# Performance work log

Hardware: AMD Instinct MI355X
Metric: run time of the kernel (lower is better)

The kernel has to match this reference:

```python
import jax, jax.numpy as jnp
import numpy as np

B, T, N, F, CH = 64, 8, 2000, 16, 64  # batch, timesteps(=receptive field), nodes, in features, channels (h_dim//2)
TASK = CH          # task_dim = h_dim // 2
P_TREAT = 0.5      # args.p
P1 = 1.0           # args.p1
BN_EPS = 1e-5


def setup_inputs() -> dict:
    key = jax.random.key(0)
    ks = jax.random.split(key, 40)
    def rn(i, shape, s=0.1):
        return jax.random.normal(ks[i], shape, dtype=jnp.float32) * s
    return {
        "X": jax.random.normal(ks[0], (B, T, N, F), dtype=jnp.float32),
        "A": jax.random.uniform(ks[1], (N, N), dtype=jnp.float32),
        "C": jax.random.randint(ks[2], (B, N), 0, 2, dtype=jnp.int32),
        "Y": jax.random.uniform(ks[3], (B, N), dtype=jnp.float32),
        "Cc": jnp.zeros((B, N), jnp.float32),
        "start_w": rn(4, (CH, F)),
        "start_b": rn(5, (CH,), 0.01),
        "filt_w": rn(6, (3, CH, CH, 2)),
        "filt_b": rn(7, (3, CH), 0.01),
        "gate_w": rn(8, (3, CH, CH, 2)),
        "gate_b": rn(9, (3, CH), 0.01),
        "skip_w": rn(10, (3, CH, CH)),
        "skip_b": rn(11, (3, CH), 0.01),
        "bn_g": 1.0 + rn(12, (3, CH), 0.01),
        "bn_b": rn(13, (3, CH), 0.01),
        "nodevec1": jax.random.normal(ks[14], (N, 10), dtype=jnp.float32),
        "nodevec2": jax.random.normal(ks[15], (10, N), dtype=jnp.float32),
        "task_emb": rn(16, (TASK,)),
        "gcn_w": rn(17, (CH, 3 * CH)),
        "gcn_b": rn(18, (CH,), 0.01),
        "h0_w1": rn(19, (CH, TASK + CH)),
        "h0_b1": rn(20, (CH,), 0.01),
        "h0_w2": rn(21, (1, CH)),
        "h0_b2": rn(22, (1,), 0.01),
        "h1_w1": rn(23, (CH, TASK + CH)),
        "h1_b1": rn(24, (CH,), 0.01),
        "h1_w2": rn(25, (1, CH)),
        "h1_b2": rn(26, (1,), 0.01),
    }


def _conv1x1(x, w, b):
    # x: (B,Cin,N,L), w: (Cout,Cin)
    return jnp.einsum('bcnl,oc->bonl', x, w) + b[None, :, None, None]


def _dil_conv(x, w, b, d):
    # kernel (1,2), dilation d along time, no padding -> width shrinks by d
    L = x.shape[-1]
    y = (jnp.einsum('bcnl,oc->bonl', x[..., :L - d], w[:, :, 0])
         + jnp.einsum('bcnl,oc->bonl', x[..., d:], w[:, :, 1]))
    return y + b[None, :, None, None]


def reference(X, A, C, Y, Cc, start_w, start_b, filt_w, filt_b, gate_w, gate_b,
              skip_w, skip_b, bn_g, bn_b, nodevec1, nodevec2, task_emb, gcn_w, gcn_b,
              h0_w1, h0_b1, h0_w2, h0_b2, h1_w1, h1_b1, h1_w2, h1_b2):
    x = jnp.transpose(X, (0, 3, 2, 1))            # (B,F,N,T)
    x = _conv1x1(x, start_w, start_b)             # (B,CH,N,T)
    adp = jax.nn.softmax(jax.nn.relu(nodevec1 @ nodevec2), axis=1)  # (N,N)
    skip = None
    d = 1
    for i in range(3):  # layers, dilations 1,2,4
        res = x
        f = jnp.tanh(_dil_conv(res, filt_w[i], filt_b[i], d))
        g = jax.nn.sigmoid(_dil_conv(res, gate_w[i], gate_b[i], d))
        x = f * g
        s = _conv1x1(x, skip_w[i], skip_b[i])
        skip = s if skip is None else s + skip[..., -s.shape[-1]:]
        x = x + res[..., -x.shape[-1]:]
        # eval-mode BatchNorm2d with running_mean=0, running_var=1
        scale = (bn_g[i] / jnp.sqrt(1.0 + BN_EPS))[None, :, None, None]
        x = x * scale + bn_b[i][None, :, None, None]
        d *= 2
    # gcn on skip (width 1): out = [x, A@x, A@(A@x)] -> concat -> 1x1 (dropout=eval identity)
    x1 = jnp.einsum('bcvl,vw->bcwl', skip, adp)
    x2 = jnp.einsum('bcvl,vw->bcwl', x1, adp)
    h = jnp.concatenate([skip, x1, x2], axis=1)   # (B,3CH,N,1)
    gx = jax.nn.relu(_conv1x1(h, gcn_w, gcn_b))   # (B,CH,N,1)
    bs, _, n_nodes, _ = gx.shape
    task = jnp.broadcast_to(task_emb[None, :, None, None], (bs, TASK, n_nodes, 1))
    z = jnp.concatenate([task, gx], axis=1)       # (B,TASK+CH,N,1)

    def hyp(w1, b1, w2, b2):
        hh = jax.nn.relu(_conv1x1(z, w1, b1))
        return _conv1x1(hh, w2, b2).reshape(-1)

    y1 = jax.nn.sigmoid(hyp(h1_w1, h1_b1, h1_w2, h1_b2))
    y0 = jax.nn.sigmoid(hyp(h0_w1, h0_b1, h0_w2, h0_b2))
    t = C.reshape(-1)
    y = jnp.where(t > 0, y1, y0)
    yc = jnp.clip(y, 1e-7, 1.0 - 1e-7)
    Yf = Y.reshape(-1)
    bce = -jnp.mean(Yf * jnp.log(yc) + (1.0 - Yf) * jnp.log(1.0 - yc))
    # linear MMD (mmd2_lin, CFR): masked means, jit-friendly
    zb = jnp.transpose(z, (0, 2, 1, 3)).reshape(bs * n_nodes, -1)  # (B*N, TASK+CH)
    tm = (t > 0).astype(zb.dtype)
    mean_t = (tm @ zb) / jnp.maximum(tm.sum(), 1.0)
    mean_c = ((1.0 - tm) @ zb) / jnp.maximum((1.0 - tm).sum(), 1.0)
    imb = jnp.sum((2.0 * P_TREAT * mean_t - 2.0 * (1.0 - P_TREAT) * mean_c) ** 2)
    loss = bce + P1 * imb
    return (loss, y, y0, y1)
```

## Files before the change

### kernel.cpp

```cpp
#include <hip/hip_runtime.h>
#include <cstdint>

#define NB 64
#define TT 8
#define NN 2000
#define NF 16
#define NCH 64
#define NPAD 2048
#define BCD 4096
#define ITEMS 128000

#define OFF_ADPF  0
#define OFF_ST    4194304
#define OFF_X2    0
#define OFF_ADPT  8388608
#define OFF_S     10485760
#define OFF_X1F   18874368
#define OFF_X1T   27262976
#define OFF_C01   31457280
#define OFF_WGCNT (OFF_C01 + 128)
#define OFF_W1TT  (OFF_WGCNT + 12288)
#define OFF_PART  (OFF_W1TT + 8192)
#define OFF_RED   (OFF_PART + 270336)
#define OFF_WAW   (OFF_RED + 136)
#define OFF_SWW   (OFF_WAW + 24576)
#define OFF_WSTW  (OFF_SWW + 6144)

#define SWZK(k, x) (((k) & ~63) | (((((k) >> 3) & 7) ^ ((x) & 7)) << 3) | ((k) & 7))
#define GSWZ(n) ((((n) >> 3) ^ (n)) & 7)

typedef __attribute__((ext_vector_type(8))) short short8;
typedef __attribute__((ext_vector_type(4))) float f32x4;
typedef const __attribute__((address_space(1))) uint32_t* gas_t;
typedef __attribute__((address_space(3))) uint32_t* las_t;

__device__ __forceinline__ float fast_rcp(float x) { return __builtin_amdgcn_rcpf(x); }
__device__ __forceinline__ float fast_tanh(float x) {
    x = fminf(fmaxf(x, -10.f), 10.f);
    float e = __expf(2.f * x);
    return (e - 1.f) * fast_rcp(e + 1.f);
}
__device__ __forceinline__ float fast_sigmoid(float x) {
    return fast_rcp(1.f + __expf(-x));
}
__device__ __forceinline__ unsigned short f2bf(float f) {
    uint32_t u = __float_as_uint(f);
    u += 0x7fff + ((u >> 16) & 1);
    return (unsigned short)(u >> 16);
}
__device__ __forceinline__ float bf2f(unsigned short b) {
    return __uint_as_float(((uint32_t)b) << 16);
}

__global__ __launch_bounds__(256) void prep_kernel(const float* __restrict__ gcn_w,
                            const float* __restrict__ h0_w1, const float* __restrict__ h0_b1,
                            const float* __restrict__ h1_w1, const float* __restrict__ h1_b1,
                            const float* __restrict__ task_emb,
                            const float* __restrict__ filt_w, const float* __restrict__ gate_w,
                            const float* __restrict__ skip_w, const float* __restrict__ start_w,
                            float* __restrict__ c01, float* __restrict__ wgcnT,
                            float* __restrict__ w1tT,
                            unsigned short* __restrict__ waw,
                            unsigned short* __restrict__ sww,
                            unsigned short* __restrict__ wstw)
{
    const int GS = 64 * 256;
    int gt = blockIdx.x * 256 + threadIdx.x;
    for (int idx = gt; idx < 64 * 192; idx += GS) {
        int o = idx / 192, j = idx % 192;
        wgcnT[j * 64 + o] = gcn_w[idx];
    }
    for (int idx = gt; idx < 4096; idx += GS) {
        int o = idx >> 6, c = idx & 63;
        w1tT[c * 64 + o]        = h0_w1[o * 128 + 64 + c];
        w1tT[4096 + c * 64 + o] = h1_w1[o * 128 + 64 + c];
    }
    for (int job = gt; job < 3 * 2 * 128 * 8; job += GS) {
        int L = job / 2048, rem = job % 2048;
        int p = rem >> 10, rem2 = rem & 1023;
        int r = rem2 >> 3, chp = rem2 & 7;
        int cho = chp ^ (r & 7);
        #pragma unroll
        for (int i = 0; i < 8; ++i) {
            int c = cho * 8 + i;
            float v = (r < 64) ? filt_w[L * 8192 + r * 128 + c * 2 + p]
                               : gate_w[L * 8192 + (r - 64) * 128 + c * 2 + p];
            waw[((L * 2 + p) * 128 + r) * 64 + chp * 8 + i] = f2bf(v);
        }
    }
    for (int job = gt; job < 3 * 64 * 8; job += GS) {
        int L = job / 512, rem = job % 512;
        int r = rem >> 3, chp = rem & 7;
        int cho = chp ^ (r & 7);
        #pragma unroll
        for (int i = 0; i < 8; ++i)
            sww[(L * 64 + r) * 64 + chp * 8 + i] = f2bf(skip_w[L * 4096 + r * 64 + cho * 8 + i]);
    }
    for (int job = gt; job < 64 * 8; job += GS) {
        int r = job >> 3, chp = job & 7;
        int cho = chp ^ (r & 7);
        #pragma unroll
        for (int i = 0; i < 8; ++i) {
            int k = cho * 8 + i;
            wstw[r * 64 + chp * 8 + i] = (k < 16) ? f2bf(start_w[r * 16 + k]) : (unsigned short)0;
        }
    }
    if (gt < 128) {
        int head = gt >> 6, o = gt & 63;
        const float* w1 = head ? h1_w1 : h0_w1;
        const float* b1 = head ? h1_b1 : h0_b1;
        float a = b1[o];
        for (int k = 0; k < 64; ++k) a = fmaf(w1[o * 128 + k], task_emb[k], a);
        c01[gt] = a;
    }
}

__global__ __launch_bounds__(256) void adp_kernel(const float* __restrict__ nv1,
                                                  const float* __restrict__ nv2,
                                                  float* __restrict__ adpF)
{
    __shared__ float nv1s[10];
    __shared__ float rbuf[4];
    int tid = threadIdx.x;
    int r = blockIdx.x;
    if (tid < 10) nv1s[tid] = nv1[r * 10 + tid];
    __syncthreads();

    float val[8];
    float vmax = -3.4e38f;
    #pragma unroll
    for (int s = 0; s < 8; ++s) {
        int j = tid + s * 256;
        if (j < NN) {
            float v = 0.f;
            #pragma unroll
            for (int k = 0; k < 10; ++k) v = fmaf(nv1s[k], nv2[k * NN + j], v);
            v = fmaxf(v, 0.f);
            val[s] = v;
            vmax = fmaxf(vmax, v);
        } else val[s] = -3.4e38f;
    }
    for (int off = 32; off; off >>= 1) vmax = fmaxf(vmax, __shfl_down(vmax, off, 64));
    if ((tid & 63) == 0) rbuf[tid >> 6] = vmax;
    __syncthreads();
    vmax = fmaxf(fmaxf(rbuf[0], rbuf[1]), fmaxf(rbuf[2], rbuf[3]));
    __syncthreads();
    float sum = 0.f;
    #pragma unroll
    for (int s = 0; s < 8; ++s) {
        int j = tid + s * 256;
        if (j < NN) { val[s] = expf(val[s] - vmax); sum += val[s]; }
    }
    for (int off = 32; off; off >>= 1) sum += __shfl_down(sum, off, 64);
    if ((tid & 63) == 0) rbuf[tid >> 6] = sum;
    __syncthreads();
    sum = rbuf[0] + rbuf[1] + rbuf[2] + rbuf[3];
    float inv = 1.f / sum;
    #pragma unroll
    for (int s = 0; s < 8; ++s) {
        int j = tid + s * 256;
        if (j < NN) adpF[(size_t)r * NPAD + j] = val[s] * inv;
    }
}

__global__ __launch_bounds__(256) void transpose_adp(const float* __restrict__ adpF,
                                                     unsigned short* __restrict__ adpT)
{
    __shared__ float tile[64][65];
    int tid = threadIdx.x;
    int r0 = blockIdx.x * 64;
    int j0 = blockIdx.y * 64;
    #pragma unroll
    for (int s = 0; s < 16; ++s) {
        int idx = s * 256 + tid;
        int i = idx >> 6, jj = idx & 63;
        int r = r0 + i, j = j0 + jj;
        tile[i][jj] = (r < NN && j < NN) ? adpF[(size_t)r * NPAD + j] : 0.f;
    }
    __syncthreads();
    #pragma unroll
    for (int s = 0; s < 2; ++s) {
        int slot = s * 256 + tid;
        int j = slot >> 3, ch = slot & 7;
        short8 v;
        #pragma unroll
        for (int e = 0; e < 8; ++e) v[e] = (short)f2bf(tile[ch * 8 + e][j]);
        *(short8*)&adpT[(size_t)(j0 + j) * NPAD + r0 + ((ch ^ (j & 7)) << 3)] = v;
    }
}

template<int NG, int WOUT, int D>
__device__ __forceinline__ void mfma_phaseB(int L,
    const unsigned short* __restrict__ xb, unsigned short* __restrict__ gbuf,
    const unsigned short* __restrict__ WA, const float* __restrict__ biasAll,
    int wave, int lr, int lk)
{
    if (wave >= NG) return;
    int idx = wave * 16 + lr;
    int n = (idx / WOUT) * 8 + (idx % WOUT);
    f32x4 aF[4], aG[4];
    #pragma unroll
    for (int mt = 0; mt < 4; ++mt) {
        aF[mt] = (f32x4){0.f, 0.f, 0.f, 0.f};
        aG[mt] = (f32x4){0.f, 0.f, 0.f, 0.f};
    }
    #pragma unroll
    for (int p = 0; p < 2; ++p) {
        int nb = n + p * D;
        const unsigned short* WAp = WA + p * 8192;
        #pragma unroll
        for (int ks = 0; ks < 2; ++ks) {
            short8 bv = *(const short8*)&xb[(nb * 8 + ((ks * 4 + lk) ^ (nb & 7))) * 8];
            #pragma unroll
            for (int mt = 0; mt < 4; ++mt) {
                int r = mt * 16 + lr;
                short8 av = *(const short8*)&WAp[(r * 8 + ((ks * 4 + lk) ^ (r & 7))) * 8];
                aF[mt] = __builtin_amdgcn_mfma_f32_16x16x32_bf16(av, bv, aF[mt], 0, 0, 0);
            }
            #pragma unroll
            for (int mt = 0; mt < 4; ++mt) {
                int r = (mt + 4) * 16 + lr;
                short8 av = *(const short8*)&WAp[(r * 8 + ((ks * 4 + lk) ^ (r & 7))) * 8];
                aG[mt] = __builtin_amdgcn_mfma_f32_16x16x32_bf16(av, bv, aG[mt], 0, 0, 0);
            }
        }
    }
    int gs = GSWZ(n);
    #pragma unroll
    for (int mt = 0; mt < 4; ++mt) {
        int ob = mt * 16 + lk * 4;
        ushort4 p;
        p.x = f2bf(fast_tanh(aF[mt][0] + biasAll[L * 128 + ob + 0]) * fast_sigmoid(aG[mt][0] + biasAll[L * 128 + 64 + ob + 0]));
        p.y = f2bf(fast_tanh(aF[mt][1] + biasAll[L * 128 + ob + 1]) * fast_sigmoid(aG[mt][1] + biasAll[L * 128 + 64 + ob + 1]));
        p.z = f2bf(fast_tanh(aF[mt][2] + biasAll[L * 128 + ob + 2]) * fast_sigmoid(aG[mt][2] + biasAll[L * 128 + 64 + ob + 2]));
        p.w = f2bf(fast_tanh(aF[mt][3] + biasAll[L * 128 + ob + 3]) * fast_sigmoid(aG[mt][3] + biasAll[L * 128 + 64 + ob + 3]));
        *(ushort4*)&gbuf[((n * 8) + ((mt * 2 + (lk >> 1)) ^ gs)) * 8 + (lk & 1) * 4] = p;
    }
}

template<int L, int D, int WOUT>
__device__ __forceinline__ void phaseC_conv(unsigned short* __restrict__ xb,
    const unsigned short* __restrict__ gbuf,
    const float* __restrict__ bn_g, const float* __restrict__ bn_b,
    float xreg[2][8], int wave, int o)
{
    float bsc = bn_g[L * 64 + o] * rsqrtf(1.0f + 1e-5f);
    float bsh = bn_b[L * 64 + o];
    #pragma unroll
    for (int gi = 0; gi < 2; ++gi) {
        int g = wave * 2 + gi;
        #pragma unroll
        for (int t = 0; t < WOUT; ++t) {
            int n = g * 8 + t;
            float gv = bf2f(gbuf[(n * 8 + ((o >> 3) ^ GSWZ(n))) * 8 + (o & 7)]);
            float nx = (gv + xreg[gi][t + D]) * bsc + bsh;
            xreg[gi][t] = nx;
            xb[(n * 8 + ((o >> 3) ^ (n & 7))) * 8 + (o & 7)] = f2bf(nx);
        }
    }
}

__device__ __forceinline__ void phaseC_skip(int LASTT,
    const unsigned short* __restrict__ gbuf, const unsigned short* __restrict__ SW,
    f32x4 skacc[4], int wave, int lr, int lk)
{
    if (wave >= 2) return;
    int g = wave * 16 + lr;
    int n = g * 8 + LASTT;
    int gs = GSWZ(n);
    #pragma unroll
    for (int ks = 0; ks < 2; ++ks) {
        short8 bv = *(const short8*)&gbuf[(n * 8 + ((ks * 4 + lk) ^ gs)) * 8];
        #pragma unroll
        for (int mt = 0; mt < 4; ++mt) {
            int r = mt * 16 + lr;
            short8 av = *(const short8*)&SW[(r * 8 + ((ks * 4 + lk) ^ (r & 7))) * 8];
            skacc[mt] = __builtin_amdgcn_mfma_f32_16x16x32_bf16(av, bv, skacc[mt], 0, 0, 0);
        }
    }
}

__global__ __launch_bounds__(1024) void temporal_kernel(
    const float* __restrict__ X,
    const float* __restrict__ start_b,
    const unsigned short* __restrict__ waw,
    const unsigned short* __restrict__ sww,
    const unsigned short* __restrict__ wstw,
    const float* __restrict__ filt_b, const float* __restrict__ gate_b,
    const float* __restrict__ skip_b,
    const float* __restrict__ bn_g, const float* __restrict__ bn_b,
    float* __restrict__ S, unsigned short* __restrict__ St)
{
    extern __shared__ float smem[];
    unsigned short* xb   = (unsigned short*)smem;
    unsigned short* gbuf = (unsigned short*)(smem + 8192);
    unsigned short* WA   = (unsigned short*)(smem + 16384);
    unsigned short* SW   = (unsigned short*)(smem + 24576);
    float* biasAll       = smem + 26624;

    int tid = threadIdx.x;
    int wave = tid >> 6, lane = tid & 63;
    int lr = lane & 15, lk = lane >> 4;
    int o = lane;
    int item0 = blockIdx.x * 32;

    if (tid < 512)
        __builtin_amdgcn_global_load_lds((gas_t)(wstw + tid * 8), (las_t)(WA + tid * 8), 16, 0, 0);
    if (tid < 384) {
        int L = tid >> 7, oo = tid & 127;
        biasAll[tid] = (oo < 64) ? filt_b[L * 64 + oo] : gate_b[L * 64 + oo - 64];
    }
    #pragma unroll
    for (int s = 0; s < 2; ++s) {
        int idx = s * 1024 + tid;
        int n = idx >> 3, c = idx & 7;
        int g = n >> 3, t = n & 7;
        int ig = item0 + g, b = ig / NN, nn = ig - b * NN;
        int cho = c ^ (n & 7);
        short8 v = {0, 0, 0, 0, 0, 0, 0, 0};
        if (cho < 2) {
            const float* src = &X[((size_t)(b * TT + t) * NN + nn) * NF + cho * 8];
            float4 f0 = *(const float4*)src;
            float4 f1 = *(const float4*)(src + 4);
            v[0] = (short)f2bf(f0.x); v[1] = (short)f2bf(f0.y);
            v[2] = (short)f2bf(f0.z); v[3] = (short)f2bf(f0.w);
            v[4] = (short)f2bf(f1.x); v[5] = (short)f2bf(f1.y);
            v[6] = (short)f2bf(f1.z); v[7] = (short)f2bf(f1.w);
        }
        *(short8*)&xb[(n * 8 + c) * 8] = v;
    }
    __syncthreads();

    {
        f32x4 aS[4];
        #pragma unroll
        for (int mt = 0; mt < 4; ++mt) aS[mt] = (f32x4){0.f, 0.f, 0.f, 0.f};
        int n = wave * 16 + lr;
        short8 bv = *(const short8*)&xb[(n * 8 + (lk ^ (n & 7))) * 8];
        #pragma unroll
        for (int mt = 0; mt < 4; ++mt) {
            int r = mt * 16 + lr;
            short8 av = *(const short8*)&WA[(r * 8 + (lk ^ (r & 7))) * 8];
            aS[mt] = __builtin_amdgcn_mfma_f32_16x16x32_bf16(av, bv, aS[mt], 0, 0, 0);
        }
        int gs = GSWZ(n);
        #pragma unroll
        for (int mt = 0; mt < 4; ++mt) {
            ushort4 p;
            p.x = f2bf(aS[mt][0]); p.y = f2bf(aS[mt][1]);
            p.z = f2bf(aS[mt][2]); p.w = f2bf(aS[mt][3]);
            *(ushort4*)&gbuf[((n * 8) + ((mt * 2 + (lk >> 1)) ^ gs)) * 8 + (lk & 1) * 4] = p;
        }
    }
    if (tid < 512)
        __builtin_amdgcn_global_load_lds((gas_t)(sww + tid * 8), (las_t)(SW + tid * 8), 16, 0, 0);
    __syncthreads();

    float xreg[2][8];
    f32x4 skacc[4];
    #pragma unroll
    for (int mt = 0; mt < 4; ++mt) skacc[mt] = (f32x4){0.f, 0.f, 0.f, 0.f};

    {
        __builtin_amdgcn_global_load_lds((gas_t)(waw + (size_t)tid * 8),
                                         (las_t)(WA + tid * 8), 16, 0, 0);
        __builtin_amdgcn_global_load_lds((gas_t)(waw + (size_t)(tid + 1024) * 8),
                                         (las_t)(WA + (tid + 1024) * 8), 16, 0, 0);
        float sb = start_b[o];
        #pragma unroll
        for (int gi = 0; gi < 2; ++gi) {
            int g = wave * 2 + gi;
            #pragma unroll
            for (int t = 0; t < 8; ++t) {
                int n = g * 8 + t;
                float gv = bf2f(gbuf[(n * 8 + ((o >> 3) ^ GSWZ(n))) * 8 + (o & 7)]) + sb;
                xreg[gi][t] = gv;
                xb[(n * 8 + ((o >> 3) ^ (n & 7))) * 8 + (o & 7)] = f2bf(gv);
            }
        }
    }
    __syncthreads();

    mfma_phaseB<14, 7, 1>(0, xb, gbuf, WA, biasAll, wave, lr, lk);
    __syncthreads();
    phaseC_skip(6, gbuf, SW, skacc, wave, lr, lk);
    phaseC_conv<0, 1, 7>(xb, gbuf, bn_g, bn_b, xreg, wave, o);
    __builtin_amdgcn_global_load_lds((gas_t)(waw + (size_t)(16384 + tid * 8)),
                                     (las_t)(WA + tid * 8), 16, 0, 0);
    __builtin_amdgcn_global_load_lds((gas_t)(waw + (size_t)(16384 + (tid + 1024) * 8)),
                                     (las_t)(WA + (tid + 1024) * 8), 16, 0, 0);
    __syncthreads();

    mfma_phaseB<10, 5, 2>(1, xb, gbuf, WA, biasAll, wave, lr, lk);
    if (tid < 512)
        __builtin_amdgcn_global_load_lds((gas_t)(sww + (size_t)(4096 + tid * 8)),
                                         (las_t)(SW + tid * 8), 16, 0, 0);
    __syncthreads();
    phaseC_skip(4, gbuf, SW, skacc, wave, lr, lk);
    phaseC_conv<1, 2, 5>(xb, gbuf, bn_g, bn_b, xreg, wave, o);
    __builtin_amdgcn_global_load_lds((gas_t)(waw + (size_t)(32768 + tid * 8)),
                                     (las_t)(WA + tid * 8), 16, 0, 0);
    __builtin_amdgcn_global_load_lds((gas_t)(waw + (size_t)(32768 + (tid + 1024) * 8)),
                                     (las_t)(WA + (tid + 1024) * 8), 16, 0, 0);
    __syncthreads();

    mfma_phaseB<2, 1, 4>(2, xb, gbuf, WA, biasAll, wave, lr, lk);
    if (tid < 512)
        __builtin_amdgcn_global_load_lds((gas_t)(sww + (size_t)(8192 + tid * 8)),
                                         (las_t)(SW + tid * 8), 16, 0, 0);
    __syncthreads();
    phaseC_skip(0, gbuf, SW, skacc, wave, lr, lk);

    if (wave < 2) {
        int g = wave * 16 + lr;
        int ig = item0 + g, b = ig / NN, nn = ig - b * NN;
        #pragma unroll
        for (int mt = 0; mt < 4; ++mt) {
            #pragma unroll
            for (int j = 0; j < 4; ++j) {
                int oo = mt * 16 + lk * 4 + j;
                float v = skacc[mt][j] + skip_b[oo] + skip_b[64 + oo] + skip_b[128 + oo];
                int bc = b * 64 + oo;
                S[(size_t)nn * BCD + bc] = v;
                St[(size_t)bc * NPAD + SWZK(nn, oo)] = f2bf(v);
            }
        }
    }
}

__global__ __launch_bounds__(256) void gemm_mfma(
    const unsigned short* __restrict__ A, const unsigned short* __restrict__ B,
    float* __restrict__ Cf, unsigned short* __restrict__ Ct)
{
    __shared__ unsigned short As[128 * 64];
    __shared__ unsigned short Bs[128 * 64];
    int tid = threadIdx.x;
    int wave = tid >> 6, lane = tid & 63;
    int lk = lane >> 4, lr = lane & 15;
    int lid = blockIdx.x;
    int lid2 = (lid & 7) * 64 + (lid >> 3);
    int bx = lid2 & 31, by = lid2 >> 5;
    int n0 = bx * 128, m0 = by * 128;
    int wm = wave >> 1, wn = wave & 1;

    f32x4 acc[4][4];
    #pragma unroll
    for (int i = 0; i < 4; ++i)
        #pragma unroll
        for (int j = 0; j < 4; ++j)
            acc[i][j] = (f32x4){0.f, 0.f, 0.f, 0.f};

    for (int k0 = 0; k0 < NPAD; k0 += 64) {
        #pragma unroll
        for (int i = 0; i < 4; ++i) {
            int chunk = wave * 4 + i;
            int row = chunk * 8 + (lane >> 3);
            int koff = (lane & 7) * 8;
            __builtin_amdgcn_global_load_lds(
                (gas_t)(A + (size_t)(m0 + row) * NPAD + k0 + koff),
                (las_t)(&As[chunk * 512]), 16, 0, 0);
            __builtin_amdgcn_global_load_lds(
                (gas_t)(B + (size_t)(n0 + row) * NPAD + k0 + koff),
                (las_t)(&Bs[chunk * 512]), 16, 0, 0);
        }
        __syncthreads();
        #pragma unroll
        for (int s = 0; s < 2; ++s) {
            short8 av[4], bv[4];
            #pragma unroll
            for (int f = 0; f < 4; ++f) {
                int m = wm * 64 + f * 16 + lr;
                int ca = ((s * 4 + lk) ^ (m & 7));
                av[f] = *(const short8*)&As[m * 64 + ca * 8];
                int n = wn * 64 + f * 16 + lr;
                int cb = ((s * 4 + lk) ^ (n & 7));
                bv[f] = *(const short8*)&Bs[n * 64 + cb * 8];
            }
            #pragma unroll
            for (int fi = 0; fi < 4; ++fi)
                #pragma unroll
                for (int fj = 0; fj < 4; ++fj)
                    acc[fi][fj] = __builtin_amdgcn_mfma_f32_16x16x32_bf16(
                        av[fi], bv[fj], acc[fi][fj], 0, 0, 0);
        }
        __syncthreads();
    }

    #pragma unroll
    for (int fi = 0; fi < 4; ++fi) {
        #pragma unroll
        for (int fj = 0; fj < 4; ++fj) {
            int m = m0 + wm * 64 + fi * 16 + lk * 4;
            int n = n0 + wn * 64 + fj * 16 + lr;
            f32x4 v = acc[fi][fj];
            if (Cf) {
                Cf[(size_t)(m + 0) * BCD + n] = v[0];
                Cf[(size_t)(m + 1) * BCD + n] = v[1];
                Cf[(size_t)(m + 2) * BCD + n] = v[2];
                Cf[(size_t)(m + 3) * BCD + n] = v[3];
            }
            if (Ct) {
                ushort4 p;
                p.x = f2bf(v[0]); p.y = f2bf(v[1]);
                p.z = f2bf(v[2]); p.w = f2bf(v[3]);
                *(ushort4*)&Ct[(size_t)n * NPAD + SWZK(m, n)] = p;
            }
        }
    }
}

__global__ __launch_bounds__(256) void head_kernel(
    const float* __restrict__ S, const float* __restrict__ x1f,
    const float* __restrict__ x2,
    const float* __restrict__ wgcnT, const float* __restrict__ gcn_b,
    const float* __restrict__ c01, const float* __restrict__ w1tT,
    const float* __restrict__ h0_w2, const float* __restrict__ h0_b2,
    const float* __restrict__ h1_w2, const float* __restrict__ h1_b2,
    const int* __restrict__ Ct, const float* __restrict__ Yf,
    float* __restrict__ out, float* __restrict__ partials)
{
    __shared__ float hl[4][4][192];
    __shared__ float gxl[4][4][64];
    int tid = threadIdx.x;
    int wave = tid >> 6, o = tid & 63;
    int wid = blockIdx.x * 4 + wave;
    float w2a = h0_w2[o], w2b = h1_w2[o];
    float b20 = h0_b2[0], b21 = h1_b2[0];
    float cb = gcn_b[o], c0a = c01[o], c0b = c01[64 + o];

    float accT = 0.f, accC = 0.f, bce = 0.f, cT = 0.f, cC = 0.f;

    for (int base = wid * 4; base < ITEMS; base += 2048 * 4) {
        #pragma unroll
        for (int it = 0; it < 4; ++it) {
            int item = base + it;
            int b = item / NN, n = item - b * NN;
            int bc = b * 64 + o;
            hl[wave][it][o]       = S[(size_t)n * BCD + bc];
            hl[wave][it][64 + o]  = x1f[(size_t)n * BCD + bc];
            hl[wave][it][128 + o] = x2[(size_t)n * BCD + bc];
        }
        float a0 = cb, a1 = cb, a2 = cb, a3 = cb;
        for (int j = 0; j < 192; ++j) {
            float w = wgcnT[j * 64 + o];
            a0 = fmaf(w, hl[wave][0][j], a0);
            a1 = fmaf(w, hl[wave][1][j], a1);
            a2 = fmaf(w, hl[wave][2][j], a2);
            a3 = fmaf(w, hl[wave][3][j], a3);
        }
        float gxv[4] = {fmaxf(a0, 0.f), fmaxf(a1, 0.f), fmaxf(a2, 0.f), fmaxf(a3, 0.f)};
        #pragma unroll
        for (int it = 0; it < 4; ++it) gxl[wave][it][o] = gxv[it];

        float p0[4], p1[4];
        #pragma unroll
        for (int it = 0; it < 4; ++it) { p0[it] = c0a; p1[it] = c0b; }
        for (int c = 0; c < 64; ++c) {
            float w0 = w1tT[c * 64 + o];
            float w1 = w1tT[4096 + c * 64 + o];
            float g0 = gxl[wave][0][c], g1 = gxl[wave][1][c];
            float g2 = gxl[wave][2][c], g3 = gxl[wave][3][c];
            p0[0] = fmaf(w0, g0, p0[0]); p0[1] = fmaf(w0, g1, p0[1]);
            p0[2] = fmaf(w0, g2, p0[2]); p0[3] = fmaf(w0, g3, p0[3]);
            p1[0] = fmaf(w1, g0, p1[0]); p1[1] = fmaf(w1, g1, p1[1]);
            p1[2] = fmaf(w1, g2, p1[2]); p1[3] = fmaf(w1, g3, p1[3]);
        }
        #pragma unroll
        for (int it = 0; it < 4; ++it) {
            float r0 = w2a * fmaxf(p0[it], 0.f);
            float r1 = w2b * fmaxf(p1[it], 0.f);
            #pragma unroll
            for (int off = 32; off; off >>= 1) {
                r0 += __shfl_down(r0, off, 64);
                r1 += __shfl_down(r1, off, 64);
            }
            int item = base + it;
            int tt = Ct[item];
            if (o == 0) {
                float y0 = 1.f / (1.f + expf(-(r0 + b20)));
                float y1 = 1.f / (1.f + expf(-(r1 + b21)));
                float y = (tt > 0) ? y1 : y0;
                out[1 + item] = y;
                out[1 + ITEMS + item] = y0;
                out[1 + 2 * ITEMS + item] = y1;
                float yc = fminf(fmaxf(y, 1e-7f), 1.f - 1e-7f);
                float Yv = Yf[item];
                bce -= Yv * logf(yc) + (1.f - Yv) * logf(1.f - yc);
                if (tt > 0) cT += 1.f; else cC += 1.f;
            }
            if (tt > 0) accT += gxv[it]; else accC += gxv[it];
        }
    }
    partials[wid * 132 + o] = accT;
    partials[wid * 132 + 64 + o] = accC;
    if (o == 0) {
        partials[wid * 132 + 128] = bce;
        partials[wid * 132 + 129] = cT;
        partials[wid * 132 + 130] = cC;
    }
}

__global__ __launch_bounds__(256) void reduce_kernel(const float* __restrict__ partials,
                                                     float* __restrict__ red)
{
    __shared__ float rb[4];
    int slot = blockIdx.x;
    int tid = threadIdx.x;
    float s = 0.f;
    for (int w = tid; w < 2048; w += 256) s += partials[w * 132 + slot];
    #pragma unroll
    for (int off = 32; off; off >>= 1) s += __shfl_down(s, off, 64);
    if ((tid & 63) == 0) rb[tid >> 6] = s;
    __syncthreads();
    if (tid == 0) red[slot] = rb[0] + rb[1] + rb[2] + rb[3];
}

__global__ void final_kernel(const float* __restrict__ red,
                             const float* __restrict__ task_emb,
                             float* __restrict__ out)
{
    int tid = threadIdx.x;
    float cT = red[129], cC = red[130];
    float iT = 1.f / fmaxf(cT, 1.f), iC = 1.f / fmaxf(cC, 1.f);
    float d1 = task_emb[tid] * (cT * iT) - task_emb[tid] * (cC * iC);
    float d2 = red[tid] * iT - red[64 + tid] * iC;
    float p = d1 * d1 + d2 * d2;
    #pragma unroll
    for (int off = 32; off; off >>= 1) p += __shfl_down(p, off, 64);
    if (tid == 0) out[0] = red[128] * (1.f / (float)ITEMS) + p;
}

extern "C" void kernel_launch(void* const* d_in, const int* in_sizes, int n_in,
                              void* d_out, int out_size, void* d_ws, size_t ws_size,
                              hipStream_t stream)
{
    const float* X       = (const float*)d_in[0];
    const int*   Ct      = (const int*)d_in[2];
    const float* Yf      = (const float*)d_in[3];
    const float* start_w = (const float*)d_in[5];
    const float* start_b = (const float*)d_in[6];
    const float* filt_w  = (const float*)d_in[7];
    const float* filt_b  = (const float*)d_in[8];
    const float* gate_w  = (const float*)d_in[9];
    const float* gate_b  = (const float*)d_in[10];
    const float* skip_w  = (const float*)d_in[11];
    const float* skip_b  = (const float*)d_in[12];
    const float* bn_g    = (const float*)d_in[13];
    const float* bn_b    = (const float*)d_in[14];
    const float* nv1     = (const float*)d_in[15];
    const float* nv2     = (const float*)d_in[16];
    const float* task    = (const float*)d_in[17];
    const float* gcn_w   = (const float*)d_in[18];
    const float* gcn_b   = (const float*)d_in[19];
    const float* h0_w1   = (const float*)d_in[20];
    const float* h0_b1   = (const float*)d_in[21];
    const float* h0_w2   = (const float*)d_in[22];
    const float* h0_b2   = (const float*)d_in[23];
    const float* h1_w1   = (const float*)d_in[24];
    const float* h1_b1   = (const float*)d_in[25];
    const float* h1_w2   = (const float*)d_in[26];
    const float* h1_b2   = (const float*)d_in[27];

    float* ws    = (float*)d_ws;
    float* adpF  = ws + OFF_ADPF;
    unsigned short* St   = (unsigned short*)(ws + OFF_ST);
    float* x2    = ws + OFF_X2;
    unsigned short* adpT = (unsigned short*)(ws + OFF_ADPT);
    float* S     = ws + OFF_S;
    float* x1f   = ws + OFF_X1F;
    unsigned short* x1t  = (unsigned short*)(ws + OFF_X1T);
    float* c01   = ws + OFF_C01;
    float* wgcnT = ws + OFF_WGCNT;
    float* w1tT  = ws + OFF_W1TT;
    float* part  = ws + OFF_PART;
    float* red   = ws + OFF_RED;
    unsigned short* waw  = (unsigned short*)(ws + OFF_WAW);
    unsigned short* sww  = (unsigned short*)(ws + OFF_SWW);
    unsigned short* wstw = (unsigned short*)(ws + OFF_WSTW);
    float* outp  = (float*)d_out;

    hipMemsetAsync(St, 0, (size_t)BCD * NPAD * sizeof(unsigned short), stream);

    prep_kernel<<<64, 256, 0, stream>>>(gcn_w, h0_w1, h0_b1, h1_w1, h1_b1, task,
                                        filt_w, gate_w, skip_w, start_w,
                                        c01, wgcnT, w1tT, waw, sww, wstw);
    adp_kernel<<<NN, 256, 0, stream>>>(nv1, nv2, adpF);
    dim3 tg(NPAD / 64, NPAD / 64);
    transpose_adp<<<tg, 256, 0, stream>>>(adpF, adpT);

    const int K2_LDS = 27008 * 4;
    hipFuncSetAttribute(reinterpret_cast<const void*>(temporal_kernel),
                        hipFuncAttributeMaxDynamicSharedMemorySize, K2_LDS);
    temporal_kernel<<<ITEMS / 32, 1024, K2_LDS, stream>>>(
        X, start_b, waw, sww, wstw, filt_b, gate_b,
        skip_b, bn_g, bn_b, S, St);

    gemm_mfma<<<512, 256, 0, stream>>>(adpT, St, x1f, x1t);
    gemm_mfma<<<512, 256, 0, stream>>>(adpT, x1t, x2, nullptr);

    head_kernel<<<512, 256, 0, stream>>>(S, x1f, x2, wgcnT, gcn_b, c01, w1tT,
                                         h0_w2, h0_b2, h1_w2, h1_b2,
                                         Ct, Yf, outp, part);
    reduce_kernel<<<131, 256, 0, stream>>>(part, red);
    final_kernel<<<1, 64, 0, stream>>>(red, task, outp);
}
```

Before: 544.0 us.

## Split temporal kernel into two half-tiles and ping-pong their phases across waves

The temporal kernel now splits its 32 items into two 16-item halves with separate LDS activation and gate buffers. Different waves run the MFMA gated conv of one half while others do the skip/residual/BN update of the other half, which cuts the number of idle waves per barrier. Weights are double-buffered (WA0/WA1), and all skip weights are preloaded once at kernel start. LDS usage rises from about 108KB to about 157KB per block, and the schedule becomes more intricate, with more barriers overall.

```diff
diff --git a/kernel.cpp b/kernel.cpp
--- a/kernel.cpp
+++ b/kernel.cpp
@@ -94,7 +94,7 @@
         int cho = chp ^ (r & 7);
         #pragma unroll
         for (int i = 0; i < 8; ++i)
-            sww[(L * 64 + r) * 64 + chp * 8 + i] = f2bf(skip_w[L * 4096 + r * 64 + cho * 8 + i]);
+            sww[((L * 64 + r) * 8 + chp) * 8 + i] = f2bf(skip_w[L * 4096 + r * 64 + cho * 8 + i]);
     }
     for (int job = gt; job < 64 * 8; job += GS) {
         int r = job >> 3, chp = job & 7;
@@ -189,14 +189,14 @@
     }
 }
 
-template<int NG, int WOUT, int D>
+template<int NG, int WOUT, int D, int WBASE>
 __device__ __forceinline__ void mfma_phaseB(int L,
     const unsigned short* __restrict__ xb, unsigned short* __restrict__ gbuf,
     const unsigned short* __restrict__ WA, const float* __restrict__ biasAll,
     int wave, int lr, int lk)
 {
-    if (wave >= NG) return;
-    int idx = wave * 16 + lr;
+    if (wave < WBASE || wave >= WBASE + NG) return;
+    int idx = (wave - WBASE) * 16 + lr;
     int n = (idx / WOUT) * 8 + (idx % WOUT);
     f32x4 aF[4], aG[4];
     #pragma unroll
@@ -242,31 +242,27 @@
 __device__ __forceinline__ void phaseC_conv(unsigned short* __restrict__ xb,
     const unsigned short* __restrict__ gbuf,
     const float* __restrict__ bn_g, const float* __restrict__ bn_b,
-    float xreg[2][8], int wave, int o)
+    float xreg[8], int wave, int o)
 {
     float bsc = bn_g[L * 64 + o] * rsqrtf(1.0f + 1e-5f);
     float bsh = bn_b[L * 64 + o];
-    #pragma unroll
-    for (int gi = 0; gi < 2; ++gi) {
-        int g = wave * 2 + gi;
-        #pragma unroll
-        for (int t = 0; t < WOUT; ++t) {
-            int n = g * 8 + t;
-            float gv = bf2f(gbuf[(n * 8 + ((o >> 3) ^ GSWZ(n))) * 8 + (o & 7)]);
-            float nx = (gv + xreg[gi][t + D]) * bsc + bsh;
-            xreg[gi][t] = nx;
-            xb[(n * 8 + ((o >> 3) ^ (n & 7))) * 8 + (o & 7)] = f2bf(nx);
-        }
-    }
-}
-
-__device__ __forceinline__ void phaseC_skip(int LASTT,
+    int g = wave;
+    #pragma unroll
+    for (int t = 0; t < WOUT; ++t) {
+        int n = g * 8 + t;
+        float gv = bf2f(gbuf[(n * 8 + ((o >> 3) ^ GSWZ(n))) * 8 + (o & 7)]);
+        float nx = (gv + xreg[t + D]) * bsc + bsh;
+        xreg[t] = nx;
+        xb[(n * 8 + ((o >> 3) ^ (n & 7))) * 8 + (o & 7)] = f2bf(nx);
+    }
+}
+
+__device__ __forceinline__ void phaseC_skip(int L, int LASTT, int SWAVE,
     const unsigned short* __restrict__ gbuf, const unsigned short* __restrict__ SW,
     f32x4 skacc[4], int wave, int lr, int lk)
 {
-    if (wave >= 2) return;
-    int g = wave * 16 + lr;
-    int n = g * 8 + LASTT;
+    if (wave != SWAVE) return;
+    int n = lr * 8 + LASTT;
     int gs = GSWZ(n);
     #pragma unroll
     for (int ks = 0; ks < 2; ++ks) {
@@ -274,8 +270,28 @@
         #pragma unroll
         for (int mt = 0; mt < 4; ++mt) {
             int r = mt * 16 + lr;
-            short8 av = *(const short8*)&SW[(r * 8 + ((ks * 4 + lk) ^ (r & 7))) * 8];
+            short8 av = *(const short8*)&SW[((L * 64 + r) * 8 + ((ks * 4 + lk) ^ (r & 7))) * 8];
             skacc[mt] = __builtin_amdgcn_mfma_f32_16x16x32_bf16(av, bv, skacc[mt], 0, 0, 0);
+        }
+    }
+}
+
+__device__ __forceinline__ void final_write(int FWAVE, int TOFS, int item0,
+    const f32x4 skacc[4], const float* __restrict__ skip_b,
+    float* __restrict__ S, unsigned short* __restrict__ St,
+    int wave, int lr, int lk)
+{
+    if (wave != FWAVE) return;
+    int ig = item0 + TOFS + lr, b = ig / NN, nn = ig - b * NN;
+    #pragma unroll
+    for (int mt = 0; mt < 4; ++mt) {
+        #pragma unroll
+        for (int j = 0; j < 4; ++j) {
+            int oo = mt * 16 + lk * 4 + j;
+            float v = skacc[mt][j] + skip_b[oo] + skip_b[64 + oo] + skip_b[128 + oo];
+            int bc = b * 64 + oo;
+            S[(size_t)nn * BCD + bc] = v;
+            St[(size_t)bc * NPAD + SWZK(nn, oo)] = f2bf(v);
         }
     }
 }
@@ -292,11 +308,14 @@
     float* __restrict__ S, unsigned short* __restrict__ St)
 {
     extern __shared__ float smem[];
-    unsigned short* xb   = (unsigned short*)smem;
-    unsigned short* gbuf = (unsigned short*)(smem + 8192);
-    unsigned short* WA   = (unsigned short*)(smem + 16384);
-    unsigned short* SW   = (unsigned short*)(smem + 24576);
-    float* biasAll       = smem + 26624;
+    unsigned short* xbA   = (unsigned short*)smem;
+    unsigned short* xbB   = (unsigned short*)(smem + 4096);
+    unsigned short* gbufA = (unsigned short*)(smem + 8192);
+    unsigned short* gbufB = (unsigned short*)(smem + 12288);
+    unsigned short* WA0   = (unsigned short*)(smem + 16384);
+    unsigned short* WA1   = (unsigned short*)(smem + 24576);
+    unsigned short* SW    = (unsigned short*)(smem + 32768);
+    float* biasAll        = smem + 38912;
 
     int tid = threadIdx.x;
     int wave = tid >> 6, lane = tid & 63;
@@ -305,7 +324,9 @@
     int item0 = blockIdx.x * 32;
 
     if (tid < 512)
-        __builtin_amdgcn_global_load_lds((gas_t)(wstw + tid * 8), (las_t)(WA + tid * 8), 16, 0, 0);
+        __builtin_amdgcn_global_load_lds((gas_t)(wstw + tid * 8), (las_t)(WA0 + tid * 8), 16, 0, 0);
+    for (int idx = tid; idx < 1536; idx += 1024)
+        __builtin_amdgcn_global_load_lds((gas_t)(sww + idx * 8), (las_t)(SW + idx * 8), 16, 0, 0);
     if (tid < 384) {
         int L = tid >> 7, oo = tid & 127;
         biasAll[tid] = (oo < 64) ? filt_b[L * 64 + oo] : gate_b[L * 64 + oo - 64];
@@ -313,10 +334,13 @@
     #pragma unroll
     for (int s = 0; s < 2; ++s) {
         int idx = s * 1024 + tid;
-        int n = idx >> 3, c = idx & 7;
-        int g = n >> 3, t = n & 7;
-        int ig = item0 + g, b = ig / NN, nn = ig - b * NN;
-        int cho = c ^ (n & 7);
+        int ng = idx >> 3, c = idx & 7;
+        int gg = ng >> 3, t = ng & 7;
+        int tl = gg >> 4;
+        int nl = (gg & 15) * 8 + t;
+        unsigned short* xbt = tl ? xbB : xbA;
+        int ig = item0 + gg, b = ig / NN, nn = ig - b * NN;
+        int cho = c ^ (nl & 7);
         short8 v = {0, 0, 0, 0, 0, 0, 0, 0};
         if (cho < 2) {
             const float* src = &X[((size_t)(b * TT + t) * NN + nn) * NF + cho * 8];
@@ -327,105 +351,99 @@
             v[4] = (short)f2bf(f1.x); v[5] = (short)f2bf(f1.y);
             v[6] = (short)f2bf(f1.z); v[7] = (short)f2bf(f1.w);
         }
-        *(short8*)&xb[(n * 8 + c) * 8] = v;
+        *(short8*)&xbt[(nl * 8 + c) * 8] = v;
     }
     __syncthreads();
 
     {
+        int nglob = wave * 16 + lr;
+        int tl = nglob >> 7, nl = nglob & 127;
+        const unsigned short* xbt = tl ? xbB : xbA;
+        unsigned short* gbt = tl ? gbufB : gbufA;
         f32x4 aS[4];
         #pragma unroll
         for (int mt = 0; mt < 4; ++mt) aS[mt] = (f32x4){0.f, 0.f, 0.f, 0.f};
-        int n = wave * 16 + lr;
-        short8 bv = *(const short8*)&xb[(n * 8 + (lk ^ (n & 7))) * 8];
+        short8 bv = *(const short8*)&xbt[(nl * 8 + (lk ^ (nl & 7))) * 8];
         #pragma unroll
         for (int mt = 0; mt < 4; ++mt) {
             int r = mt * 16 + lr;
-            short8 av = *(const short8*)&WA[(r * 8 + (lk ^ (r & 7))) * 8];
+            short8 av = *(const short8*)&WA0[(r * 8 + (lk ^ (r & 7))) * 8];
             aS[mt] = __builtin_amdgcn_mfma_f32_16x16x32_bf16(av, bv, aS[mt], 0, 0, 0);
         }
-        int gs = GSWZ(n);
+        int gs = GSWZ(nl);
         #pragma unroll
         for (int mt = 0; mt < 4; ++mt) {
             ushort4 p;
             p.x = f2bf(aS[mt][0]); p.y = f2bf(aS[mt][1]);
             p.z = f2bf(aS[mt][2]); p.w = f2bf(aS[mt][3]);
-            *(ushort4*)&gbuf[((n * 8) + ((mt * 2 + (lk >> 1)) ^ gs)) * 8 + (lk & 1) * 4] = p;
-        }
-    }
-    if (tid < 512)
-        __builtin_amdgcn_global_load_lds((gas_t)(sww + tid * 8), (las_t)(SW + tid * 8), 16, 0, 0);
-    __syncthreads();
-
-    float xreg[2][8];
+            *(ushort4*)&gbt[((nl * 8) + ((mt * 2 + (lk >> 1)) ^ gs)) * 8 + (lk & 1) * 4] = p;
+        }
+        __builtin_amdgcn_global_load_lds((gas_t)(waw + (size_t)tid * 8),
+                                         (las_t)(WA1 + tid * 8), 16, 0, 0);
+        __builtin_amdgcn_global_load_lds((gas_t)(waw + (size_t)(tid + 1024) * 8),
+                                         (las_t)(WA1 + (tid + 1024) * 8), 16, 0, 0);
+    }
+    __syncthreads();
+
+    float xregA[8], xregB[8];
     f32x4 skacc[4];
     #pragma unroll
     for (int mt = 0; mt < 4; ++mt) skacc[mt] = (f32x4){0.f, 0.f, 0.f, 0.f};
 
     {
-        __builtin_amdgcn_global_load_lds((gas_t)(waw + (size_t)tid * 8),
-                                         (las_t)(WA + tid * 8), 16, 0, 0);
-        __builtin_amdgcn_global_load_lds((gas_t)(waw + (size_t)(tid + 1024) * 8),
-                                         (las_t)(WA + (tid + 1024) * 8), 16, 0, 0);
         float sb = start_b[o];
         #pragma unroll
-        for (int gi = 0; gi < 2; ++gi) {
-            int g = wave * 2 + gi;
-            #pragma unroll
-            for (int t = 0; t < 8; ++t) {
-                int n = g * 8 + t;
-                float gv = bf2f(gbuf[(n * 8 + ((o >> 3) ^ GSWZ(n))) * 8 + (o & 7)]) + sb;
-                xreg[gi][t] = gv;
-                xb[(n * 8 + ((o >> 3) ^ (n & 7))) * 8 + (o & 7)] = f2bf(gv);
-            }
-        }
-    }
-    __syncthreads();
-
-    mfma_phaseB<14, 7, 1>(0, xb, gbuf, WA, biasAll, wave, lr, lk);
-    __syncthreads();
-    phaseC_skip(6, gbuf, SW, skacc, wave, lr, lk);
-    phaseC_conv<0, 1, 7>(xb, gbuf, bn_g, bn_b, xreg, wave, o);
-    __builtin_amdgcn_global_load_lds((gas_t)(waw + (size_t)(16384 + tid * 8)),
-                                     (las_t)(WA + tid * 8), 16, 0, 0);
-    __builtin_amdgcn_global_load_lds((gas_t)(waw + (size_t)(16384 + (tid + 1024) * 8)),
-                                     (las_t)(WA + (tid + 1024) * 8), 16, 0, 0);
-    __syncthreads();
-
-    mfma_phaseB<10, 5, 2>(1, xb, gbuf, WA, biasAll, wave, lr, lk);
-    if (tid < 512)
-        __builtin_amdgcn_global_load_lds((gas_t)(sww + (size_t)(4096 + tid * 8)),
-                                         (las_t)(SW + tid * 8), 16, 0, 0);
-    __syncthreads();
-    phaseC_skip(4, gbuf, SW, skacc, wave, lr, lk);
-    phaseC_conv<1, 2, 5>(xb, gbuf, bn_g, bn_b, xreg, wave, o);
-    __builtin_amdgcn_global_load_lds((gas_t)(waw + (size_t)(32768 + tid * 8)),
-                                     (las_t)(WA + tid * 8), 16, 0, 0);
-    __builtin_amdgcn_global_load_lds((gas_t)(waw + (size_t)(32768 + (tid + 1024) * 8)),
-                                     (las_t)(WA + (tid + 1024) * 8), 16, 0, 0);
-    __syncthreads();
-
-    mfma_phaseB<2, 1, 4>(2, xb, gbuf, WA, biasAll, wave, lr, lk);
-    if (tid < 512)
-        __builtin_amdgcn_global_load_lds((gas_t)(sww + (size_t)(8192 + tid * 8)),
-                                         (las_t)(SW + tid * 8), 16, 0, 0);
-    __syncthreads();
-    phaseC_skip(0, gbuf, SW, skacc, wave, lr, lk);
-
-    if (wave < 2) {
-        int g = wave * 16 + lr;
-        int ig = item0 + g, b = ig / NN, nn = ig - b * NN;
-        #pragma unroll
-        for (int mt = 0; mt < 4; ++mt) {
-            #pragma unroll
-            for (int j = 0; j < 4; ++j) {
-                int oo = mt * 16 + lk * 4 + j;
-                float v = skacc[mt][j] + skip_b[oo] + skip_b[64 + oo] + skip_b[128 + oo];
-                int bc = b * 64 + oo;
-                S[(size_t)nn * BCD + bc] = v;
-                St[(size_t)bc * NPAD + SWZK(nn, oo)] = f2bf(v);
-            }
-        }
-    }
+        for (int t = 0; t < 8; ++t) {
+            int n = wave * 8 + t;
+            int ls = (n * 8 + ((o >> 3) ^ GSWZ(n))) * 8 + (o & 7);
+            int xs = (n * 8 + ((o >> 3) ^ (n & 7))) * 8 + (o & 7);
+            float gA = bf2f(gbufA[ls]) + sb;
+            float gB = bf2f(gbufB[ls]) + sb;
+            xregA[t] = gA; xregB[t] = gB;
+            xbA[xs] = f2bf(gA);
+            xbB[xs] = f2bf(gB);
+        }
+    }
+    __syncthreads();
+
+    mfma_phaseB<7, 7, 1, 0>(0, xbA, gbufA, WA1, biasAll, wave, lr, lk);
+    __builtin_amdgcn_global_load_lds((gas_t)(waw + (size_t)(2048 + tid) * 8),
+                                     (las_t)(WA0 + tid * 8), 16, 0, 0);
+    __builtin_amdgcn_global_load_lds((gas_t)(waw + (size_t)(2048 + tid + 1024) * 8),
+                                     (las_t)(WA0 + (tid + 1024) * 8), 16, 0, 0);
+    __syncthreads();
+
+    mfma_phaseB<7, 7, 1, 9>(0, xbB, gbufB, WA1, biasAll, wave, lr, lk);
+    phaseC_skip(0, 6, 0, gbufA, SW, skacc, wave, lr, lk);
+    phaseC_conv<0, 1, 7>(xbA, gbufA, bn_g, bn_b, xregA, wave, o);
+    __syncthreads();
+
+    mfma_phaseB<5, 5, 2, 7>(1, xbA, gbufA, WA0, biasAll, wave, lr, lk);
+    phaseC_skip(0, 6, 1, gbufB, SW, skacc, wave, lr, lk);
+    phaseC_conv<0, 1, 7>(xbB, gbufB, bn_g, bn_b, xregB, wave, o);
+    __builtin_amdgcn_global_load_lds((gas_t)(waw + (size_t)(4096 + tid) * 8),
+                                     (las_t)(WA1 + tid * 8), 16, 0, 0);
+    __builtin_amdgcn_global_load_lds((gas_t)(waw + (size_t)(4096 + tid + 1024) * 8),
+                                     (las_t)(WA1 + (tid + 1024) * 8), 16, 0, 0);
+    __syncthreads();
+
+    mfma_phaseB<5, 5, 2, 2>(1, xbB, gbufB, WA0, biasAll, wave, lr, lk);
+    phaseC_skip(1, 4, 0, gbufA, SW, skacc, wave, lr, lk);
+    phaseC_conv<1, 2, 5>(xbA, gbufA, bn_g, bn_b, xregA, wave, o);
+    __syncthreads();
+
+    mfma_phaseB<1, 1, 4, 12>(2, xbA, gbufA, WA1, biasAll, wave, lr, lk);
+    phaseC_skip(1, 4, 1, gbufB, SW, skacc, wave, lr, lk);
+    phaseC_conv<1, 2, 5>(xbB, gbufB, bn_g, bn_b, xregB, wave, o);
+    __syncthreads();
+
+    mfma_phaseB<1, 1, 4, 15>(2, xbB, gbufB, WA1, biasAll, wave, lr, lk);
+    phaseC_skip(2, 0, 0, gbufA, SW, skacc, wave, lr, lk);
+    final_write(0, 0, item0, skacc, skip_b, S, St, wave, lr, lk);
+    __syncthreads();
+
+    phaseC_skip(2, 0, 1, gbufB, SW, skacc, wave, lr, lk);
+    final_write(1, 16, item0, skacc, skip_b, S, St, wave, lr, lk);
 }
 
 __global__ __launch_bounds__(256) void gemm_mfma(
@@ -688,7 +706,7 @@
     dim3 tg(NPAD / 64, NPAD / 64);
     transpose_adp<<<tg, 256, 0, stream>>>(adpF, adpT);
 
-    const int K2_LDS = 27008 * 4;
+    const int K2_LDS = 39296 * 4;
     hipFuncSetAttribute(reinterpret_cast<const void*>(temporal_kernel),
                         hipFuncAttributeMaxDynamicSharedMemorySize, K2_LDS);
     temporal_kernel<<<ITEMS / 32, 1024, K2_LDS, stream>>>(
```

Result: slower. 589.0 us (+8.3%).
